# Optimization experiments

Measured on AMD Instinct MI355X. Metric: run time of the kernel, lower is better.

Reference implementation:

```python
import jax, jax.numpy as jnp
import numpy as np

D_MODEL = 1024
N_SEQ = 2048
H = 16


def _rope_tables(d, n_seq):
    # theta_i = 10000^(-2i/d), i in [0, d/2)
    i = jnp.arange(d // 2, dtype=jnp.float32)
    theta = jnp.power(10000.0, -2.0 * i / d)                 # [d/2]
    ang = jnp.arange(n_seq, dtype=jnp.float32)[:, None] * theta[None, :]  # [S, d/2]
    cos = jnp.repeat(jnp.cos(ang), 2, axis=-1)               # [S, d] (cos duplicated per pair)
    s = jnp.sin(ang)
    sin = jnp.stack([s, -s], axis=-1).reshape(n_seq, d)      # [S, d] (+sin, -sin interleaved)
    return cos, sin


def _apply_rope(x, cos, sin):
    d = x.shape[-1]
    # swap adjacent pairs: (x0,x1,x2,x3,...) -> (x1,x0,x3,x2,...)
    x2 = x.reshape(x.shape[:-1] + (d // 2, 2))[..., ::-1].reshape(x.shape)
    return x * cos + x2 * sin


def setup_inputs() -> dict:
    key = jax.random.key(0)
    ks = jax.random.split(key, 8)
    B, S, D = 2, N_SEQ, D_MODEL
    scale = 1.0 / np.sqrt(D)
    return {
        "q": jax.random.normal(ks[0], (B, S, D), dtype=jnp.float32),
        "k": jax.random.normal(ks[1], (B, S, D), dtype=jnp.float32),
        "v": jax.random.normal(ks[2], (B, S, D), dtype=jnp.float32),
        "W_q": jax.random.normal(ks[3], (D, D), dtype=jnp.float32) * scale,
        "W_k": jax.random.normal(ks[4], (D, D), dtype=jnp.float32) * scale,
        "W_v": jax.random.normal(ks[5], (D, D), dtype=jnp.float32) * scale,
        "W_o": jax.random.normal(ks[6], (D, D), dtype=jnp.float32) * scale,
        "b_o": jax.random.normal(ks[7], (D,), dtype=jnp.float32) * scale,
    }


def reference(q, k, v, W_q, W_k, W_v, W_o, b_o):
    B, S, D = q.shape
    d_k = D // H
    cos, sin = _rope_tables(D, N_SEQ)

    query = _apply_rope(q @ W_q.T, cos, sin)  # RoPE over full d_model, pre head-split
    key_ = _apply_rope(k @ W_k.T, cos, sin)
    value = v @ W_v.T

    def split_heads(x):
        return x.reshape(B, S, H, d_k).transpose(0, 2, 1, 3)  # [B,H,S,dk]

    qh, kh, vh = split_heads(query), split_heads(key_), split_heads(value)

    scores = jnp.einsum("bhsd,bhtd->bhst", qh, kh) / jnp.sqrt(jnp.float32(d_k))
    attn = jax.nn.softmax(scores, axis=-1)
    y = jnp.einsum("bhst,bhtd->bhsd", attn, vh)               # [B,H,S,dk]
    y = y.transpose(0, 2, 1, 3).reshape(B, S, D)
    return y @ W_o.T + b_o
```

## Files before the change

### kernel.cpp

```cpp
#include <hip/hip_runtime.h>
#include <hip/hip_bf16.h>

using bf16 = __hip_bfloat16;
using bf16x8 = __attribute__((ext_vector_type(8))) short;
using f32x4 = __attribute__((ext_vector_type(4))) float;

#define LOG2E 1.44269504088896f

__device__ __forceinline__ void gload_lds16(const void* g, void* lds) {
    __builtin_amdgcn_global_load_lds(
        (const __attribute__((address_space(1))) void*)g,
        (__attribute__((address_space(3))) void*)lds, 16, 0, 0);
}

struct __align__(16) BH8 { bf16 h[8]; };
struct __align__(8)  BH4 { bf16 h[4]; };

struct CvtArgs { const float* src[7]; BH8* dst[7]; };

__global__ __launch_bounds__(256) void cvt_all(CvtArgs ca) {
    int i = blockIdx.x * 256 + threadIdx.x;
    const float* src; BH8* dst; int off;
    if (i < 3 * 524288) {
        int w = i >> 19; off = i & 524287;
        src = ca.src[w]; dst = ca.dst[w];
    } else {
        int j = i - 3 * 524288;
        int w = 3 + (j >> 17); off = j & 131071;
        src = ca.src[w]; dst = ca.dst[w];
    }
    const float4* p = (const float4*)src + (size_t)off * 2;
    float4 a = p[0], b = p[1];
    BH8 r;
    r.h[0] = __float2bfloat16(a.x); r.h[1] = __float2bfloat16(a.y);
    r.h[2] = __float2bfloat16(a.z); r.h[3] = __float2bfloat16(a.w);
    r.h[4] = __float2bfloat16(b.x); r.h[5] = __float2bfloat16(b.y);
    r.h[6] = __float2bfloat16(b.z); r.h[7] = __float2bfloat16(b.w);
    dst[off] = r;
}

__global__ __launch_bounds__(256) void rope_tables(float* __restrict__ ct,
                                                   float* __restrict__ st) {
    int idx = blockIdx.x * 256 + threadIdx.x;
    if (idx >= 2048 * 512) return;
    int s = idx >> 9, i = idx & 511;
    float theta = exp2f((float)i * -0.0259525632413075f);
    float ang = (float)s * theta;
    ct[idx] = cosf(ang);
    st[idx] = sinf(ang);
}

struct ProjArgs {
    const bf16* A[3];
    const bf16* W[3];
    void* out[3];
    int mode[3];
};

template <int MF>
__global__ __launch_bounds__(256, 2) void gemm_bt(ProjArgs pa,
        const float* __restrict__ ct, const float* __restrict__ st,
        const float* __restrict__ bias) {
    constexpr int Kd = 1024;
    constexpr int BM = MF * 32;
    __shared__ __align__(16) bf16 As[BM * 32];
    __shared__ __align__(16) bf16 Bs[128 * 32];
    const int z = blockIdx.z;
    const bf16* __restrict__ A = pa.A[z];
    const bf16* __restrict__ W = pa.W[z];
    const int mode = pa.mode[z];
    const int tid = threadIdx.x, wid = tid >> 6, lane = tid & 63;
    const int g = lane >> 4, l15 = lane & 15;
    const int wm = wid >> 1, wn = wid & 1;
    const int m0 = blockIdx.y * BM, n0 = blockIdx.x * 128;
    f32x4 acc[MF][4] = {};
    const int sbyte = wid * 1024 + lane * 16;

    for (int kb = 0; kb < Kd; kb += 32) {
        __syncthreads();
#pragma unroll
        for (int r = 0; r < MF / 2; ++r) {
            int byte = sbyte + r * 4096;
            int row = byte >> 6, cb = byte & 63;
            int csrc = cb ^ (((row >> 1) & 3) << 4);
            gload_lds16((const char*)(A + (size_t)(m0 + row) * Kd + kb) + csrc,
                        (char*)As + wid * 1024 + r * 4096);
        }
#pragma unroll
        for (int r = 0; r < 2; ++r) {
            int byte = sbyte + r * 4096;
            int row = byte >> 6, cb = byte & 63;
            int csrc = cb ^ (((row >> 1) & 3) << 4);
            gload_lds16((const char*)(W + (size_t)(n0 + row) * Kd + kb) + csrc,
                        (char*)Bs + wid * 1024 + r * 4096);
        }
        __syncthreads();
        bf16x8 af[MF], bw[4];
#pragma unroll
        for (int i = 0; i < MF; ++i) {
            int ra = wm * (MF * 16) + i * 16 + l15;
            af[i] = *(const bf16x8*)((const char*)As + ra * 64 +
                                     ((g * 16) ^ (((ra >> 1) & 3) << 4)));
        }
#pragma unroll
        for (int j = 0; j < 4; ++j) {
            int rb = wn * 64 + j * 16 + l15;
            bw[j] = *(const bf16x8*)((const char*)Bs + rb * 64 +
                                     ((g * 16) ^ (((rb >> 1) & 3) << 4)));
        }
#pragma unroll
        for (int i = 0; i < MF; ++i)
#pragma unroll
            for (int j = 0; j < 4; ++j)
                acc[i][j] = __builtin_amdgcn_mfma_f32_16x16x32_bf16(af[i], bw[j], acc[i][j], 0, 0, 0);
    }

    if (mode == 0) {
        float* out = (float*)pa.out[z];
#pragma unroll
        for (int i = 0; i < MF; ++i) {
            int row = m0 + wm * (MF * 16) + i * 16 + g * 4;
#pragma unroll
            for (int j = 0; j < 4; ++j) {
                int col = n0 + wn * 64 + j * 16 + l15;
                float bv = bias[col];
#pragma unroll
                for (int r = 0; r < 4; ++r)
                    out[(size_t)(row + r) * 1024 + col] = acc[i][j][r] + bv;
            }
        }
    } else if (mode == 3) {
        bf16* out = (bf16*)pa.out[z];
#pragma unroll
        for (int i = 0; i < MF; ++i) {
            int m = m0 + wm * (MF * 16) + i * 16 + g * 4;
            int b = m >> 11, s = m & 2047;
#pragma unroll
            for (int j = 0; j < 4; ++j) {
                int col = n0 + wn * 64 + j * 16 + l15;
                int h = col >> 6, dv = col & 63;
                BH4 pk;
#pragma unroll
                for (int r = 0; r < 4; ++r) pk.h[r] = __float2bfloat16(acc[i][j][r]);
                *(BH4*)(out + (((size_t)(b * 16 + h)) * 64 + dv) * 2048 + s) = pk;
            }
        }
    } else {
        bf16* out = (bf16*)pa.out[z];
        float scl = (mode == 1) ? (0.125f * LOG2E) : 1.0f;
#pragma unroll
        for (int i = 0; i < MF; ++i) {
            int mrow = m0 + wm * (MF * 16) + i * 16 + g * 4;
#pragma unroll
            for (int j = 0; j < 4; ++j) {
                int col = n0 + wn * 64 + j * 16 + l15;
                int ci = col >> 1;
                float sgn = (col & 1) ? -1.0f : 1.0f;
                int h = col >> 6, dv = col & 63;
#pragma unroll
                for (int r = 0; r < 4; ++r) {
                    int m = mrow + r;
                    int b = m >> 11, s = m & 2047;
                    float vv = acc[i][j][r];
                    float pv = __shfl_xor(vv, 1);
                    float c = ct[s * 512 + ci], sn = st[s * 512 + ci];
                    float o = (vv * c + sgn * sn * pv) * scl;
                    out[(((size_t)(b * 16 + h)) * 2048 + s) * 64 + dv] = __float2bfloat16(o);
                }
            }
        }
    }
}

__global__ __launch_bounds__(128, 2) void attn_fwd(
        const bf16* __restrict__ Qh, const bf16* __restrict__ Kh,
        const bf16* __restrict__ Vt, bf16* __restrict__ Y) {
    __shared__ __align__(16) bf16 Ks[2][64 * 64];
    __shared__ __align__(16) bf16 Vs[2][64 * 64];
    const int tid = threadIdx.x, wid = tid >> 6, lane = tid & 63;
    const int g = lane >> 4, l15 = lane & 15;
    const int lin = blockIdx.y * 32 + blockIdx.x;
    const int swz = (lin & 7) * 128 + (lin >> 3);
    const int bh = swz >> 5, qt = swz & 31;
    const int q0 = qt * 64 + wid * 32;
    const bf16* Qb = Qh + (size_t)bh * 2048 * 64;
    const bf16* Kb = Kh + (size_t)bh * 2048 * 64;
    const bf16* Vb = Vt + (size_t)bh * 64 * 2048;

    bf16x8 aq[2][2];
#pragma unroll
    for (int qfr = 0; qfr < 2; ++qfr)
#pragma unroll
        for (int kk = 0; kk < 2; ++kk)
            aq[qfr][kk] = *(const bf16x8*)(Qb + (size_t)(q0 + qfr * 16 + l15) * 64 + kk * 32 + g * 8);

    bf16x8 ones;
#pragma unroll
    for (int i = 0; i < 8; ++i) ones[i] = (short)0x3F80;

    f32x4 yacc[2][4] = {};
    f32x4 lacc[2] = {};

    int srow[4], csrc[4], kphys[4];
#pragma unroll
    for (int i = 0; i < 4; ++i) {
        int byte = wid * 1024 + lane * 16 + i * 2048;
        srow[i] = byte >> 7;
        csrc[i] = (byte & 127) ^ ((srow[i] & 7) << 4);
        int L = srow[i];
        kphys[i] = ((L >> 5) << 5) + (((L >> 2) & 3) << 3) + (((L >> 4) & 1) << 2) + (L & 3);
    }

#define STAGE(T, BUF)                                                           \
    do {                                                                        \
        _Pragma("unroll")                                                       \
        for (int i = 0; i < 4; ++i) {                                           \
            gload_lds16((const char*)(Kb + (size_t)((T) * 64 + kphys[i]) * 64) + csrc[i], \
                        (char*)&Ks[BUF][0] + wid * 1024 + i * 2048);            \
            gload_lds16((const char*)(Vb + (size_t)srow[i] * 2048 + (T) * 64) + csrc[i],  \
                        (char*)&Vs[BUF][0] + wid * 1024 + i * 2048);            \
        }                                                                       \
    } while (0)

    STAGE(0, 0);

    for (int t = 0; t < 32; ++t) {
        __syncthreads();
        if (t < 31) STAGE(t + 1, (t + 1) & 1);
        const char* Kst = (const char*)&Ks[t & 1][0];
        const char* Vst = (const char*)&Vs[t & 1][0];

        f32x4 sacc[4][2] = {};
#pragma unroll
        for (int kk = 0; kk < 2; ++kk) {
            bf16x8 kf[4];
#pragma unroll
            for (int kfr = 0; kfr < 4; ++kfr)
                kf[kfr] = *(const bf16x8*)(Kst + (kfr * 16 + l15) * 128 +
                                           ((kk * 64 + g * 16) ^ ((l15 & 7) << 4)));
            __builtin_amdgcn_s_setprio(1);
#pragma unroll
            for (int kfr = 0; kfr < 4; ++kfr)
#pragma unroll
                for (int qfr = 0; qfr < 2; ++qfr)
                    sacc[kfr][qfr] = __builtin_amdgcn_mfma_f32_16x16x32_bf16(
                        kf[kfr], aq[qfr][kk], sacc[kfr][qfr], 0, 0, 0);
            __builtin_amdgcn_s_setprio(0);
        }

        bf16x8 ap[2][2];
#pragma unroll
        for (int qfr = 0; qfr < 2; ++qfr)
#pragma unroll
            for (int ch = 0; ch < 2; ++ch) {
                float e0 = exp2f(sacc[2 * ch][qfr][0]);
                float e1 = exp2f(sacc[2 * ch][qfr][1]);
                float e2 = exp2f(sacc[2 * ch][qfr][2]);
                float e3 = exp2f(sacc[2 * ch][qfr][3]);
                float f0 = exp2f(sacc[2 * ch + 1][qfr][0]);
                float f1 = exp2f(sacc[2 * ch + 1][qfr][1]);
                float f2 = exp2f(sacc[2 * ch + 1][qfr][2]);
                float f3 = exp2f(sacc[2 * ch + 1][qfr][3]);
                union { unsigned int w[4]; bf16x8 v; } u;
                asm("v_cvt_pk_bf16_f32 %0, %1, %2" : "=v"(u.w[0]) : "v"(e0), "v"(e1));
                asm("v_cvt_pk_bf16_f32 %0, %1, %2" : "=v"(u.w[1]) : "v"(e2), "v"(e3));
                asm("v_cvt_pk_bf16_f32 %0, %1, %2" : "=v"(u.w[2]) : "v"(f0), "v"(f1));
                asm("v_cvt_pk_bf16_f32 %0, %1, %2" : "=v"(u.w[3]) : "v"(f2), "v"(f3));
                ap[qfr][ch] = u.v;
                lacc[qfr] = __builtin_amdgcn_mfma_f32_16x16x32_bf16(
                    ap[qfr][ch], ones, lacc[qfr], 0, 0, 0);
            }

#pragma unroll
        for (int ch = 0; ch < 2; ++ch) {
            bf16x8 bv[4];
#pragma unroll
            for (int dn = 0; dn < 4; ++dn)
                bv[dn] = *(const bf16x8*)(Vst + (dn * 16 + l15) * 128 +
                                          ((ch * 64 + g * 16) ^ ((l15 & 7) << 4)));
            __builtin_amdgcn_s_setprio(1);
#pragma unroll
            for (int qfr = 0; qfr < 2; ++qfr)
#pragma unroll
                for (int dn = 0; dn < 4; ++dn)
                    yacc[qfr][dn] = __builtin_amdgcn_mfma_f32_16x16x32_bf16(
                        ap[qfr][ch], bv[dn], yacc[qfr][dn], 0, 0, 0);
            __builtin_amdgcn_s_setprio(0);
        }
    }
#undef STAGE

    const int b = bh >> 4, h = bh & 15;
#pragma unroll
    for (int qfr = 0; qfr < 2; ++qfr) {
#pragma unroll
        for (int r = 0; r < 4; ++r) {
            float inv = 1.0f / lacc[qfr][r];
            int s = q0 + qfr * 16 + g * 4 + r;
            bf16* yp = Y + ((size_t)(b * 2048 + s)) * 1024 + h * 64;
#pragma unroll
            for (int dn = 0; dn < 4; ++dn)
                yp[dn * 16 + l15] = __float2bfloat16(yacc[qfr][dn][r] * inv);
        }
    }
}

extern "C" void kernel_launch(void* const* d_in, const int* in_sizes, int n_in,
                              void* d_out, int out_size, void* d_ws, size_t ws_size,
                              hipStream_t stream) {
    const float* q  = (const float*)d_in[0];
    const float* k  = (const float*)d_in[1];
    const float* v  = (const float*)d_in[2];
    const float* Wq = (const float*)d_in[3];
    const float* Wk = (const float*)d_in[4];
    const float* Wv = (const float*)d_in[5];
    const float* Wo = (const float*)d_in[6];
    const float* bo = (const float*)d_in[7];

    const size_t MB = 1048576ull;
    if (ws_size < 72 * MB) return;
    char* p = (char*)d_ws;
    bf16* qb  = (bf16*)(p + 0 * MB);
    bf16* kb  = (bf16*)(p + 8 * MB);
    bf16* vb  = (bf16*)(p + 16 * MB);
    bf16* Wqb = (bf16*)(p + 24 * MB);
    bf16* Wkb = (bf16*)(p + 26 * MB);
    bf16* Wvb = (bf16*)(p + 28 * MB);
    bf16* Wob = (bf16*)(p + 30 * MB);
    bf16* Qh  = (bf16*)(p + 32 * MB);
    bf16* Kh  = (bf16*)(p + 40 * MB);
    bf16* Vt  = (bf16*)(p + 48 * MB);
    bf16* Yb  = (bf16*)(p + 56 * MB);
    float* ct = (float*)(p + 64 * MB);
    float* st = (float*)(p + 68 * MB);

    CvtArgs ca;
    ca.src[0] = q;  ca.dst[0] = (BH8*)qb;
    ca.src[1] = k;  ca.dst[1] = (BH8*)kb;
    ca.src[2] = v;  ca.dst[2] = (BH8*)vb;
    ca.src[3] = Wq; ca.dst[3] = (BH8*)Wqb;
    ca.src[4] = Wk; ca.dst[4] = (BH8*)Wkb;
    ca.src[5] = Wv; ca.dst[5] = (BH8*)Wvb;
    ca.src[6] = Wo; ca.dst[6] = (BH8*)Wob;
    cvt_all<<<8192, 256, 0, stream>>>(ca);
    rope_tables<<<4096, 256, 0, stream>>>(ct, st);

    ProjArgs pa;
    pa.A[0] = qb;  pa.A[1] = kb;  pa.A[2] = vb;
    pa.W[0] = Wqb; pa.W[1] = Wkb; pa.W[2] = Wvb;
    pa.out[0] = Qh; pa.out[1] = Kh; pa.out[2] = Vt;
    pa.mode[0] = 1; pa.mode[1] = 2; pa.mode[2] = 3;
    gemm_bt<4><<<dim3(8, 32, 3), 256, 0, stream>>>(pa, ct, st, nullptr);

    attn_fwd<<<dim3(32, 32), 128, 0, stream>>>(Qh, Kh, Vt, Yb);

    ProjArgs pf;
    pf.A[0] = Yb; pf.A[1] = Yb; pf.A[2] = Yb;
    pf.W[0] = Wob; pf.W[1] = Wob; pf.W[2] = Wob;
    pf.out[0] = d_out; pf.out[1] = d_out; pf.out[2] = d_out;
    pf.mode[0] = 0; pf.mode[1] = 0; pf.mode[2] = 0;
    gemm_bt<2><<<dim3(8, 64, 1), 256, 0, stream>>>(pf, ct, st, bo);
}
```

Before: 150.8 us.

## Merge convert and RoPE-table kernels, truncate P to bf16, drop setprio

After: 152.8 us. Within noise of the previous version (+1.4%).

```diff
diff --git a/kernel.cpp b/kernel.cpp
--- a/kernel.cpp
+++ b/kernel.cpp
@@ -13,41 +13,46 @@
         (__attribute__((address_space(3))) void*)lds, 16, 0, 0);
 }
 
+__device__ __forceinline__ unsigned int fbits(float x) {
+    union { float f; unsigned int u; } c; c.f = x; return c.u;
+}
+
 struct __align__(16) BH8 { bf16 h[8]; };
 struct __align__(8)  BH4 { bf16 h[4]; };
 
 struct CvtArgs { const float* src[7]; BH8* dst[7]; };
 
-__global__ __launch_bounds__(256) void cvt_all(CvtArgs ca) {
-    int i = blockIdx.x * 256 + threadIdx.x;
-    const float* src; BH8* dst; int off;
-    if (i < 3 * 524288) {
-        int w = i >> 19; off = i & 524287;
-        src = ca.src[w]; dst = ca.dst[w];
+__global__ __launch_bounds__(256) void cvt_rope(CvtArgs ca,
+        float* __restrict__ ct, float* __restrict__ st) {
+    int bid = blockIdx.x;
+    if (bid < 8192) {
+        int i = bid * 256 + threadIdx.x;
+        const float* src; BH8* dst; int off;
+        if (i < 3 * 524288) {
+            int w = i >> 19; off = i & 524287;
+            src = ca.src[w]; dst = ca.dst[w];
+        } else {
+            int j = i - 3 * 524288;
+            int w = 3 + (j >> 17); off = j & 131071;
+            src = ca.src[w]; dst = ca.dst[w];
+        }
+        const float4* p = (const float4*)src + (size_t)off * 2;
+        float4 a = p[0], b = p[1];
+        BH8 r;
+        r.h[0] = __float2bfloat16(a.x); r.h[1] = __float2bfloat16(a.y);
+        r.h[2] = __float2bfloat16(a.z); r.h[3] = __float2bfloat16(a.w);
+        r.h[4] = __float2bfloat16(b.x); r.h[5] = __float2bfloat16(b.y);
+        r.h[6] = __float2bfloat16(b.z); r.h[7] = __float2bfloat16(b.w);
+        dst[off] = r;
     } else {
-        int j = i - 3 * 524288;
-        int w = 3 + (j >> 17); off = j & 131071;
-        src = ca.src[w]; dst = ca.dst[w];
-    }
-    const float4* p = (const float4*)src + (size_t)off * 2;
-    float4 a = p[0], b = p[1];
-    BH8 r;
-    r.h[0] = __float2bfloat16(a.x); r.h[1] = __float2bfloat16(a.y);
-    r.h[2] = __float2bfloat16(a.z); r.h[3] = __float2bfloat16(a.w);
-    r.h[4] = __float2bfloat16(b.x); r.h[5] = __float2bfloat16(b.y);
-    r.h[6] = __float2bfloat16(b.z); r.h[7] = __float2bfloat16(b.w);
-    dst[off] = r;
-}
-
-__global__ __launch_bounds__(256) void rope_tables(float* __restrict__ ct,
-                                                   float* __restrict__ st) {
-    int idx = blockIdx.x * 256 + threadIdx.x;
-    if (idx >= 2048 * 512) return;
-    int s = idx >> 9, i = idx & 511;
-    float theta = exp2f((float)i * -0.0259525632413075f);
-    float ang = (float)s * theta;
-    ct[idx] = cosf(ang);
-    st[idx] = sinf(ang);
+        int idx = (bid - 8192) * 256 + threadIdx.x;
+        if (idx >= 2048 * 512) return;
+        int s = idx >> 9, i = idx & 511;
+        float theta = exp2f((float)i * -0.0259525632413075f);
+        float ang = (float)s * theta;
+        ct[idx] = cosf(ang);
+        st[idx] = sinf(ang);
+    }
 }
 
 struct ProjArgs {
@@ -238,14 +243,12 @@
             for (int kfr = 0; kfr < 4; ++kfr)
                 kf[kfr] = *(const bf16x8*)(Kst + (kfr * 16 + l15) * 128 +
                                            ((kk * 64 + g * 16) ^ ((l15 & 7) << 4)));
-            __builtin_amdgcn_s_setprio(1);
 #pragma unroll
             for (int kfr = 0; kfr < 4; ++kfr)
 #pragma unroll
                 for (int qfr = 0; qfr < 2; ++qfr)
                     sacc[kfr][qfr] = __builtin_amdgcn_mfma_f32_16x16x32_bf16(
                         kf[kfr], aq[qfr][kk], sacc[kfr][qfr], 0, 0, 0);
-            __builtin_amdgcn_s_setprio(0);
         }
 
         bf16x8 ap[2][2];
@@ -262,10 +265,10 @@
                 float f2 = exp2f(sacc[2 * ch + 1][qfr][2]);
                 float f3 = exp2f(sacc[2 * ch + 1][qfr][3]);
                 union { unsigned int w[4]; bf16x8 v; } u;
-                asm("v_cvt_pk_bf16_f32 %0, %1, %2" : "=v"(u.w[0]) : "v"(e0), "v"(e1));
-                asm("v_cvt_pk_bf16_f32 %0, %1, %2" : "=v"(u.w[1]) : "v"(e2), "v"(e3));
-                asm("v_cvt_pk_bf16_f32 %0, %1, %2" : "=v"(u.w[2]) : "v"(f0), "v"(f1));
-                asm("v_cvt_pk_bf16_f32 %0, %1, %2" : "=v"(u.w[3]) : "v"(f2), "v"(f3));
+                u.w[0] = __builtin_amdgcn_perm(fbits(e1), fbits(e0), 0x07060302u);
+                u.w[1] = __builtin_amdgcn_perm(fbits(e3), fbits(e2), 0x07060302u);
+                u.w[2] = __builtin_amdgcn_perm(fbits(f1), fbits(f0), 0x07060302u);
+                u.w[3] = __builtin_amdgcn_perm(fbits(f3), fbits(f2), 0x07060302u);
                 ap[qfr][ch] = u.v;
                 lacc[qfr] = __builtin_amdgcn_mfma_f32_16x16x32_bf16(
                     ap[qfr][ch], ones, lacc[qfr], 0, 0, 0);
@@ -278,14 +281,12 @@
             for (int dn = 0; dn < 4; ++dn)
                 bv[dn] = *(const bf16x8*)(Vst + (dn * 16 + l15) * 128 +
                                           ((ch * 64 + g * 16) ^ ((l15 & 7) << 4)));
-            __builtin_amdgcn_s_setprio(1);
 #pragma unroll
             for (int qfr = 0; qfr < 2; ++qfr)
 #pragma unroll
                 for (int dn = 0; dn < 4; ++dn)
                     yacc[qfr][dn] = __builtin_amdgcn_mfma_f32_16x16x32_bf16(
                         ap[qfr][ch], bv[dn], yacc[qfr][dn], 0, 0, 0);
-            __builtin_amdgcn_s_setprio(0);
         }
     }
 #undef STAGE
@@ -342,8 +343,7 @@
     ca.src[4] = Wk; ca.dst[4] = (BH8*)Wkb;
     ca.src[5] = Wv; ca.dst[5] = (BH8*)Wvb;
     ca.src[6] = Wo; ca.dst[6] = (BH8*)Wob;
-    cvt_all<<<8192, 256, 0, stream>>>(ca);
-    rope_tables<<<4096, 256, 0, stream>>>(ct, st);
+    cvt_rope<<<12288, 256, 0, stream>>>(ca, ct, st);
 
     ProjArgs pa;
     pa.A[0] = qb;  pa.A[1] = kb;  pa.A[2] = vb;
```
